# Performance work log

Measured on AMD Instinct MI355X. Metric: run time of the kernel, lower is better.

The kernel has to match this reference:

```python
import jax, jax.numpy as jnp
import numpy as np

N_A = 50000   # 'user' nodes
N_B = 50000   # 'item' nodes
E = 1000000   # edges per relation
IN, HID, OUT = 128, 128, 64


def setup_inputs() -> dict:
    key = jax.random.key(0)
    ks = jax.random.split(key, 24)
    def glorot(k, shape):
        scale = 1.0 / np.sqrt(shape[0])
        return jax.random.normal(k, shape, jnp.float32) * scale
    inp = {
        "feat_A": jax.random.normal(ks[0], (N_A, IN), jnp.float32),
        "feat_B": jax.random.normal(ks[1], (N_B, IN), jnp.float32),
        "rates_src": jax.random.randint(ks[2], (E,), 0, N_A, jnp.int32),
        "rates_dst": jax.random.randint(ks[3], (E,), 0, N_B, jnp.int32),
        "ratedby_src": jax.random.randint(ks[4], (E,), 0, N_B, jnp.int32),
        "ratedby_dst": jax.random.randint(ks[5], (E,), 0, N_A, jnp.int32),
        "follows_src": jax.random.randint(ks[6], (E,), 0, N_A, jnp.int32),
        "follows_dst": jax.random.randint(ks[7], (E,), 0, N_A, jnp.int32),
        "neg_src": jax.random.randint(ks[8], (E,), 0, N_A, jnp.int32),
        "neg_dst": jax.random.randint(ks[9], (E,), 0, N_B, jnp.int32),
        "W1_rates": glorot(ks[10], (IN, HID)),   "b1_rates": jnp.zeros((HID,), jnp.float32),
        "W1_ratedby": glorot(ks[11], (IN, HID)), "b1_ratedby": jnp.zeros((HID,), jnp.float32),
        "W1_follows": glorot(ks[12], (IN, HID)), "b1_follows": jnp.zeros((HID,), jnp.float32),
        "W2_rates": glorot(ks[13], (HID, OUT)),   "b2_rates": jnp.zeros((OUT,), jnp.float32),
        "W2_ratedby": glorot(ks[14], (HID, OUT)), "b2_ratedby": jnp.zeros((OUT,), jnp.float32),
        "W2_follows": glorot(ks[15], (HID, OUT)), "b2_follows": jnp.zeros((OUT,), jnp.float32),
    }
    return inp


def _graph_conv(x_src, W, b, src, dst, n_src, n_dst):
    # DGL GraphConv, norm='both': D_dst^{-1/2} A D_src^{-1/2} (X W) + b
    ones = jnp.ones(src.shape[0], x_src.dtype)
    deg_out = jnp.maximum(jax.ops.segment_sum(ones, src, num_segments=n_src), 1.0)
    deg_in = jnp.maximum(jax.ops.segment_sum(ones, dst, num_segments=n_dst), 1.0)
    h = (x_src * (deg_out ** -0.5)[:, None]) @ W          # [n_src, d_out]
    agg = jax.ops.segment_sum(h[src], dst, num_segments=n_dst)  # SpMM
    return agg * (deg_in ** -0.5)[:, None] + b


def reference(feat_A, feat_B,
              W1_rates, b1_rates, W1_ratedby, b1_ratedby, W1_follows, b1_follows,
              W2_rates, b2_rates, W2_ratedby, b2_ratedby, W2_follows, b2_follows,
              rates_src, rates_dst, ratedby_src, ratedby_dst,
              follows_src, follows_dst, neg_src, neg_dst):
    # --- RGCN layer 1 (HeteroGraphConv, aggregate='sum') ---
    hB = _graph_conv(feat_A, W1_rates, b1_rates, rates_src, rates_dst, N_A, N_B)
    hA = (_graph_conv(feat_B, W1_ratedby, b1_ratedby, ratedby_src, ratedby_dst, N_B, N_A)
          + _graph_conv(feat_A, W1_follows, b1_follows, follows_src, follows_dst, N_A, N_A))
    hA = jax.nn.relu(hA)
    hB = jax.nn.relu(hB)
    # --- RGCN layer 2 ---
    oB = _graph_conv(hA, W2_rates, b2_rates, rates_src, rates_dst, N_A, N_B)
    oA = (_graph_conv(hB, W2_ratedby, b2_ratedby, ratedby_src, ratedby_dst, N_B, N_A)
          + _graph_conv(hA, W2_follows, b2_follows, follows_src, follows_dst, N_A, N_A))
    # --- HeteroInnerProduct (u_dot_v on etype 'rates') for pos and neg graphs ---
    pos_score = jnp.sum(oA[rates_src] * oB[rates_dst], axis=1, keepdims=True)  # [E, 1]
    neg_score = jnp.sum(oA[neg_src] * oB[neg_dst], axis=1, keepdims=True)      # [E, 1]
    return pos_score, neg_score
```

## Files before the change

kernel.cpp:

```cpp
#include <hip/hip_runtime.h>
#include <hip/hip_fp16.h>
#include <cstddef>
#include <type_traits>

#define N_NODES 50000
#define E_EDGES 1000000
#define NBUCK 196
#define ACHUNK 3907
#define MTILES 3125
#define HB 96
#define HCHUNK 10417
#define GB1 384
#define GB2 256

typedef _Float16 f16x8 __attribute__((ext_vector_type(8)));
typedef float f32x4 __attribute__((ext_vector_type(4)));

__global__ __launch_bounds__(256) void fused0(
        const float* __restrict__ w0, const float* __restrict__ w1,
        const float* __restrict__ w2, const float* __restrict__ w3,
        const float* __restrict__ w4, const float* __restrict__ w5,
        __half* __restrict__ Wt,
        const int* __restrict__ rs, const int* __restrict__ rd,
        const int* __restrict__ bs, const int* __restrict__ bd,
        const int* __restrict__ fs, const int* __restrict__ fd,
        int* __restrict__ bphist) {
    int bx = blockIdx.x;
    if (bx < 6 * HB) {
        __shared__ int l[NBUCK];
        int arr = bx / HB, blk = bx % HB;
        const int* idx = arr == 0 ? rs : arr == 1 ? rd : arr == 2 ? bs
                       : arr == 3 ? bd : arr == 4 ? fs : fd;
        for (int b = threadIdx.x; b < NBUCK; b += 256) l[b] = 0;
        __syncthreads();
        int e0 = blk * HCHUNK;
        int e1 = e0 + HCHUNK; if (e1 > E_EDGES) e1 = E_EDGES;
        for (int i = e0 + threadIdx.x; i < e1; i += 256)
            atomicAdd(&l[((unsigned)idx[i]) >> 8], 1);
        __syncthreads();
        int* dst = bphist + (size_t)(arr * HB + blk) * NBUCK;
        for (int b = threadIdx.x; b < NBUCK; b += 256) dst[b] = l[b];
        return;
    }
    bx -= 6 * HB;
    int m = bx / 16, part = bx % 16;
    const float* W = m == 0 ? w0 : m == 1 ? w1 : m == 2 ? w2 : m == 3 ? w3 : m == 4 ? w4 : w5;
    __half* Tt = Wt + (m < 3 ? m * 16384 : 49152 + (m - 3) * 8192);
    int ncol = m < 3 ? 128 : 64;
    int tot = 128 * ncol;
    for (int i = part * 256 + threadIdx.x; i < tot; i += 16 * 256) {
        int n = i >> 7, k = i & 127;
        Tt[i] = __float2half(W[k * ncol + n]);
    }
}

__global__ void bucket_scan_par(const int* __restrict__ bphist, int* __restrict__ gbase,
                                int* __restrict__ gcur) {
    int arr = blockIdx.x;
    int t = threadIdx.x;
    int c = 0;
    if (t < NBUCK) {
        const int* p = bphist + (size_t)arr * HB * NBUCK + t;
#pragma unroll 8
        for (int blk = 0; blk < HB; blk++) c += p[(size_t)blk * NBUCK];
    }
    int lane = t & 63, wid = t >> 6;
    __shared__ int wsum[4];
    int v = c;
#pragma unroll
    for (int o = 1; o < 64; o <<= 1) { int u = __shfl_up(v, o); if (lane >= o) v += u; }
    if (lane == 63) wsum[wid] = v;
    __syncthreads();
    int base = 0;
    for (int ww = 0; ww < wid; ww++) base += wsum[ww];
    int excl = base + v - c;
    if (t < NBUCK) {
        gbase[arr * (NBUCK + 1) + t] = excl;
        gcur[arr * NBUCK + t] = excl;
    }
    if (t == 255) gbase[arr * (NBUCK + 1) + NBUCK] = base + v;
}

__global__ __launch_bounds__(256) void fused_bin(
        const int* __restrict__ rs, const int* __restrict__ rd,
        const int* __restrict__ bs, const int* __restrict__ bd,
        const int* __restrict__ fs, const int* __restrict__ fd,
        int* __restrict__ gcur, unsigned* __restrict__ pairs,
        unsigned char* __restrict__ sbytes) {
    int y = blockIdx.y;
    __shared__ int lcnt[NBUCK];
    __shared__ int lbase[NBUCK];
    int e0 = blockIdx.x * ACHUNK;
    int e1 = e0 + ACHUNK; if (e1 > E_EDGES) e1 = E_EDGES;
    for (int b = threadIdx.x; b < NBUCK; b += 256) lcnt[b] = 0;
    __syncthreads();
    if (y < 3) {
        int rel = y, arr = 2 * rel + 1;
        const int* src = rel == 0 ? rs : rel == 1 ? bs : fs;
        const int* dst = rel == 0 ? rd : rel == 1 ? bd : fd;
        for (int i = e0 + threadIdx.x; i < e1; i += 256)
            atomicAdd(&lcnt[((unsigned)dst[i]) >> 8], 1);
        __syncthreads();
        for (int b = threadIdx.x; b < NBUCK; b += 256) {
            lbase[b] = lcnt[b] ? atomicAdd(&gcur[arr * NBUCK + b], lcnt[b]) : 0;
            lcnt[b] = 0;
        }
        __syncthreads();
        unsigned* pp = pairs + (size_t)rel * E_EDGES;
        for (int i = e0 + threadIdx.x; i < e1; i += 256) {
            int d = dst[i];
            int b = ((unsigned)d) >> 8;
            int p = lbase[b] + atomicAdd(&lcnt[b], 1);
            pp[p] = ((unsigned)(d & 255) << 16) | (unsigned)src[i];
        }
    } else {
        int rel = y - 3, arr = 2 * rel;
        const int* src = rel == 0 ? rs : rel == 1 ? bs : fs;
        for (int i = e0 + threadIdx.x; i < e1; i += 256)
            atomicAdd(&lcnt[((unsigned)src[i]) >> 8], 1);
        __syncthreads();
        for (int b = threadIdx.x; b < NBUCK; b += 256) {
            lbase[b] = lcnt[b] ? atomicAdd(&gcur[arr * NBUCK + b], lcnt[b]) : 0;
            lcnt[b] = 0;
        }
        __syncthreads();
        unsigned char* sb = sbytes + (size_t)rel * E_EDGES;
        for (int i = e0 + threadIdx.x; i < e1; i += 256) {
            int s = src[i];
            int b = ((unsigned)s) >> 8;
            int p = lbase[b] + atomicAdd(&lcnt[b], 1);
            sb[p] = (unsigned char)(s & 255);
        }
    }
}

__global__ __launch_bounds__(256) void fused_finish(
        const unsigned* __restrict__ pairs, const unsigned char* __restrict__ sbytes,
        const int* __restrict__ gbase, int* __restrict__ row_ptr,
        float* __restrict__ scales, int* __restrict__ col) {
    int y = blockIdx.y, b = blockIdx.x, t = threadIdx.x;
    __shared__ int cnt[256];
    __shared__ int rowbase[256];
    __shared__ int wsum[4];
    if (y < 3) {
        int rel = y, arr = 2 * rel;
        int p0 = gbase[arr * (NBUCK + 1) + b];
        int p1 = gbase[arr * (NBUCK + 1) + b + 1];
        const unsigned char* sb = sbytes + (size_t)rel * E_EDGES;
        cnt[t] = 0;
        __syncthreads();
        for (int i = p0 + t; i < p1; i += 256)
            atomicAdd(&cnt[sb[i]], 1);
        __syncthreads();
        int node = b * 256 + t;
        if (node < N_NODES) {
            int c = cnt[t]; if (c < 1) c = 1;
            scales[(size_t)arr * N_NODES + node] = 1.0f / sqrtf((float)c);
        }
    } else {
        int rel = y - 3, arr = 2 * rel + 1;
        int gb = gbase[arr * (NBUCK + 1) + b];
        int ge = gbase[arr * (NBUCK + 1) + b + 1];
        const unsigned* pp = pairs + (size_t)rel * E_EDGES;
        cnt[t] = 0;
        __syncthreads();
        for (int i = gb + t; i < ge; i += 256)
            atomicAdd(&cnt[pp[i] >> 16], 1);
        __syncthreads();
        int lane = t & 63, wid = t >> 6;
        int c0 = cnt[t];
        int v = c0;
#pragma unroll
        for (int o = 1; o < 64; o <<= 1) { int u = __shfl_up(v, o); if (lane >= o) v += u; }
        if (lane == 63) wsum[wid] = v;
        __syncthreads();
        int base = gb;
        for (int w = 0; w < wid; w++) base += wsum[w];
        int excl = base + v - c0;
        rowbase[t] = excl;
        int node = b * 256 + t;
        if (node <= N_NODES)
            row_ptr[(size_t)rel * (N_NODES + 1) + node] = excl;
        if (node < N_NODES) {
            int c = c0; if (c < 1) c = 1;
            scales[(size_t)arr * N_NODES + node] = 1.0f / sqrtf((float)c);
        }
        cnt[t] = 0;
        __syncthreads();
        int* cl = col + (size_t)rel * E_EDGES;
        for (int i = gb + t; i < ge; i += 256) {
            unsigned p = pp[i];
            int dl = p >> 16;
            int slot = rowbase[dl] + atomicAdd(&cnt[dl], 1);
            cl[slot] = (int)(p & 0xFFFFu);
        }
    }
}

template <int NCOL, typename XT>
__device__ __forceinline__ void gemm_body(const XT* __restrict__ X,
                                          const float* __restrict__ sc,
                                          const __half* __restrict__ Wt,
                                          __half* __restrict__ T,
                                          int bxr, int nblocks) {
    constexpr int NHALF = NCOL / 64;
    int gw = bxr * 4 + ((int)threadIdx.x >> 6);
    int lane = threadIdx.x & 63;
    int half_id = gw % NHALF;
    int mstream = gw / NHALF;
    int nstreams = nblocks * 4 / NHALF;
    int l15 = lane & 15, g = lane >> 4;

    f16x8 b[4][4];
    {
        const __half* wb = Wt + ((size_t)half_id * 64 + l15) * 128 + g * 8;
#pragma unroll
        for (int nt = 0; nt < 4; nt++)
#pragma unroll
            for (int kb = 0; kb < 4; kb++)
                b[nt][kb] = *(const f16x8*)(wb + nt * 16 * 128 + kb * 32);
    }

    for (int mt = mstream; mt < MTILES; mt += nstreams) {
        int m0 = mt * 16;
        f16x8 a[4];
        if constexpr (std::is_same<XT, float>::value) {
            const float* xr = X + (size_t)(m0 + l15) * 128 + g * 8;
#pragma unroll
            for (int kb = 0; kb < 4; kb++) {
                float4 u = *(const float4*)(xr + kb * 32);
                float4 v = *(const float4*)(xr + kb * 32 + 4);
                f16x8 t;
                t[0] = (_Float16)u.x; t[1] = (_Float16)u.y;
                t[2] = (_Float16)u.z; t[3] = (_Float16)u.w;
                t[4] = (_Float16)v.x; t[5] = (_Float16)v.y;
                t[6] = (_Float16)v.z; t[7] = (_Float16)v.w;
                a[kb] = t;
            }
        } else {
            const _Float16* xr = (const _Float16*)X + (size_t)(m0 + l15) * 128 + g * 8;
#pragma unroll
            for (int kb = 0; kb < 4; kb++)
                a[kb] = *(const f16x8*)(xr + kb * 32);
        }
        f32x4 acc[4];
#pragma unroll
        for (int nt = 0; nt < 4; nt++) acc[nt] = (f32x4){0.f, 0.f, 0.f, 0.f};
#pragma unroll
        for (int kb = 0; kb < 4; kb++)
#pragma unroll
            for (int nt = 0; nt < 4; nt++)
                acc[nt] = __builtin_amdgcn_mfma_f32_16x16x32_f16(a[kb], b[nt][kb], acc[nt], 0, 0, 0);
        int mrow = m0 + g * 4;
#pragma unroll
        for (int j = 0; j < 4; j++) {
            float sj = sc[mrow + j];
            __half* tj = T + (size_t)(mrow + j) * NCOL + half_id * 64 + l15;
            tj[0]  = __float2half(acc[0][j] * sj);
            tj[16] = __float2half(acc[1][j] * sj);
            tj[32] = __float2half(acc[2][j] * sj);
            tj[48] = __float2half(acc[3][j] * sj);
        }
    }
}

__global__ __launch_bounds__(256) void gemm_l1(const float* __restrict__ fA,
                                               const float* __restrict__ fB,
                                               const float* __restrict__ scales,
                                               const __half* __restrict__ Wt,
                                               __half* __restrict__ T012) {
    int rel = blockIdx.x / GB1, bxr = blockIdx.x % GB1;
    const float* X = (rel == 1) ? fB : fA;
    const float* sc = scales + (rel == 0 ? 0 : rel == 1 ? 2 * N_NODES : 4 * N_NODES);
    const __half* W = Wt + rel * 16384;
    __half* T = T012 + (size_t)rel * N_NODES * 128;
    gemm_body<128, float>(X, sc, W, T, bxr, GB1);
}

__global__ __launch_bounds__(256) void gemm_l2(const __half* __restrict__ hA,
                                               const __half* __restrict__ hB,
                                               const float* __restrict__ scales,
                                               const __half* __restrict__ Wt,
                                               __half* __restrict__ Tp) {
    int rel = blockIdx.x / GB2, bxr = blockIdx.x % GB2;
    const __half* X = (rel == 1) ? hB : hA;
    const float* sc = scales + (rel == 0 ? 0 : rel == 1 ? 2 * N_NODES : 4 * N_NODES);
    const __half* W = Wt + 49152 + rel * 8192;
    __half* T = Tp + (size_t)rel * N_NODES * 64;
    gemm_body<64, __half>(X, sc, W, T, bxr, GB2);
}

__global__ __launch_bounds__(256) void spmm_l1(
        const int* __restrict__ row_ptr, const int* __restrict__ col,
        const __half* __restrict__ T012, const float* __restrict__ scales,
        const float* __restrict__ b1r, const float* __restrict__ b1rb,
        const float* __restrict__ b1f,
        __half* __restrict__ hB, __half* __restrict__ hA) {
    int w = (blockIdx.x * blockDim.x + threadIdx.x) >> 6;
    int lane = threadIdx.x & 63;
    unsigned loff = (unsigned)lane << 2;
    const char* T0 = (const char*)T012;
    const char* T1 = T0 + (size_t)N_NODES * 256;
    const char* T2 = T1 + (size_t)N_NODES * 256;
#define LDT(B, c) __half22float2(*(const __half2*)((B) + (((unsigned)(c) << 8) + loff)))
    if (w < N_NODES / 2) {
        const int* cl = col;
        int rowA = w * 2, rowB = rowA + 1;
        int eA = row_ptr[rowA], EA = row_ptr[rowA + 1];
        int eB = EA, EB = row_ptr[rowB + 1];
        float axA = 0.f, ayA = 0.f, axB = 0.f, ayB = 0.f;
        while (eA + 4 <= EA && eB + 4 <= EB) {
            int a0 = cl[eA], a1 = cl[eA+1], a2 = cl[eA+2], a3 = cl[eA+3];
            int b0 = cl[eB], b1 = cl[eB+1], b2 = cl[eB+2], b3 = cl[eB+3];
            float2 v0 = LDT(T0, a0), v1 = LDT(T0, a1), v2 = LDT(T0, a2), v3 = LDT(T0, a3);
            float2 u0 = LDT(T0, b0), u1 = LDT(T0, b1), u2 = LDT(T0, b2), u3 = LDT(T0, b3);
            axA += (v0.x + v1.x) + (v2.x + v3.x); ayA += (v0.y + v1.y) + (v2.y + v3.y);
            axB += (u0.x + u1.x) + (u2.x + u3.x); ayB += (u0.y + u1.y) + (u2.y + u3.y);
            eA += 4; eB += 4;
        }
        while (eA + 4 <= EA) {
            int a0 = cl[eA], a1 = cl[eA+1], a2 = cl[eA+2], a3 = cl[eA+3];
            float2 v0 = LDT(T0, a0), v1 = LDT(T0, a1), v2 = LDT(T0, a2), v3 = LDT(T0, a3);
            axA += (v0.x + v1.x) + (v2.x + v3.x); ayA += (v0.y + v1.y) + (v2.y + v3.y);
            eA += 4;
        }
        while (eB + 4 <= EB) {
            int b0 = cl[eB], b1 = cl[eB+1], b2 = cl[eB+2], b3 = cl[eB+3];
            float2 u0 = LDT(T0, b0), u1 = LDT(T0, b1), u2 = LDT(T0, b2), u3 = LDT(T0, b3);
            axB += (u0.x + u1.x) + (u2.x + u3.x); ayB += (u0.y + u1.y) + (u2.y + u3.y);
            eB += 4;
        }
        while (eA < EA && eB < EB) {
            float2 v = LDT(T0, cl[eA]), u = LDT(T0, cl[eB]);
            axA += v.x; ayA += v.y; axB += u.x; ayB += u.y;
            eA++; eB++;
        }
        for (; eA < EA; eA++) { float2 v = LDT(T0, cl[eA]); axA += v.x; ayA += v.y; }
        for (; eB < EB; eB++) { float2 v = LDT(T0, cl[eB]); axB += v.x; ayB += v.y; }
        float bx = b1r[2 * lane], by = b1r[2 * lane + 1];
        float sA = scales[N_NODES + rowA], sB = scales[N_NODES + rowB];
        float ox = fmaxf(fmaf(axA, sA, bx), 0.f), oy = fmaxf(fmaf(ayA, sA, by), 0.f);
        *(__half2*)(hB + (size_t)rowA * 128 + 2 * lane) = __floats2half2_rn(ox, oy);
        ox = fmaxf(fmaf(axB, sB, bx), 0.f); oy = fmaxf(fmaf(ayB, sB, by), 0.f);
        *(__half2*)(hB + (size_t)rowB * 128 + 2 * lane) = __floats2half2_rn(ox, oy);
    } else {
        int r = w - N_NODES / 2;
        const int* rp1 = row_ptr + (N_NODES + 1);
        const int* rp2 = row_ptr + 2 * (N_NODES + 1);
        const int* cl1 = col + E_EDGES;
        const int* cl2 = col + 2 * (size_t)E_EDGES;
        int e1 = rp1[r], E1 = rp1[r + 1];
        int e2 = rp2[r], E2 = rp2[r + 1];
        float a1x = 0.f, a1y = 0.f, a2x = 0.f, a2y = 0.f;
        while (e1 + 4 <= E1 && e2 + 4 <= E2) {
            int a0 = cl1[e1], a1 = cl1[e1+1], a2 = cl1[e1+2], a3 = cl1[e1+3];
            int b0 = cl2[e2], b1 = cl2[e2+1], b2 = cl2[e2+2], b3 = cl2[e2+3];
            float2 v0 = LDT(T1, a0), v1 = LDT(T1, a1), v2 = LDT(T1, a2), v3 = LDT(T1, a3);
            float2 u0 = LDT(T2, b0), u1 = LDT(T2, b1), u2 = LDT(T2, b2), u3 = LDT(T2, b3);
            a1x += (v0.x + v1.x) + (v2.x + v3.x); a1y += (v0.y + v1.y) + (v2.y + v3.y);
            a2x += (u0.x + u1.x) + (u2.x + u3.x); a2y += (u0.y + u1.y) + (u2.y + u3.y);
            e1 += 4; e2 += 4;
        }
        while (e1 + 4 <= E1) {
            int a0 = cl1[e1], a1 = cl1[e1+1], a2 = cl1[e1+2], a3 = cl1[e1+3];
            float2 v0 = LDT(T1, a0), v1 = LDT(T1, a1), v2 = LDT(T1, a2), v3 = LDT(T1, a3);
            a1x += (v0.x + v1.x) + (v2.x + v3.x); a1y += (v0.y + v1.y) + (v2.y + v3.y);
            e1 += 4;
        }
        while (e2 + 4 <= E2) {
            int b0 = cl2[e2], b1 = cl2[e2+1], b2 = cl2[e2+2], b3 = cl2[e2+3];
            float2 u0 = LDT(T2, b0), u1 = LDT(T2, b1), u2 = LDT(T2, b2), u3 = LDT(T2, b3);
            a2x += (u0.x + u1.x) + (u2.x + u3.x); a2y += (u0.y + u1.y) + (u2.y + u3.y);
            e2 += 4;
        }
        while (e1 < E1 && e2 < E2) {
            float2 v = LDT(T1, cl1[e1]), u = LDT(T2, cl2[e2]);
            a1x += v.x; a1y += v.y; a2x += u.x; a2y += u.y;
            e1++; e2++;
        }
        for (; e1 < E1; e1++) { float2 v = LDT(T1, cl1[e1]); a1x += v.x; a1y += v.y; }
        for (; e2 < E2; e2++) { float2 v = LDT(T2, cl2[e2]); a2x += v.x; a2y += v.y; }
        float s1 = scales[3 * N_NODES + r], s2 = scales[5 * N_NODES + r];
        float ox = a1x * s1 + a2x * s2 + b1rb[2 * lane] + b1f[2 * lane];
        float oy = a1y * s1 + a2y * s2 + b1rb[2 * lane + 1] + b1f[2 * lane + 1];
        ox = fmaxf(ox, 0.f); oy = fmaxf(oy, 0.f);
        *(__half2*)(hA + (size_t)r * 128 + 2 * lane) = __floats2half2_rn(ox, oy);
    }
#undef LDT
}

__global__ __launch_bounds__(256) void spmm_l2(
        const int* __restrict__ row_ptr, const int* __restrict__ col,
        const __half* __restrict__ Tp, const float* __restrict__ scales,
        const float* __restrict__ b2r, const float* __restrict__ b2rb,
        const float* __restrict__ b2f,
        __half* __restrict__ oB, __half* __restrict__ oA) {
    int g = (blockIdx.x * blockDim.x + threadIdx.x) >> 5;
    int l2 = threadIdx.x & 31;
    unsigned loff = (unsigned)l2 << 2;
    const char* T0 = (const char*)Tp;
    const char* T1 = T0 + (size_t)N_NODES * 128;
    const char* T2 = T1 + (size_t)N_NODES * 128;
#define LDT(B, c) __half22float2(*(const __half2*)((B) + (((unsigned)(c) << 7) + loff)))
    if (g < N_NODES / 2) {
        const int* cl = col;
        int rowA = g * 2, rowB = rowA + 1;
        int eA = row_ptr[rowA], EA = row_ptr[rowA + 1];
        int eB = EA, EB = row_ptr[rowB + 1];
        float axA = 0.f, ayA = 0.f, axB = 0.f, ayB = 0.f;
        while (eA + 4 <= EA && eB + 4 <= EB) {
            int a0 = cl[eA], a1 = cl[eA+1], a2 = cl[eA+2], a3 = cl[eA+3];
            int b0 = cl[eB], b1 = cl[eB+1], b2 = cl[eB+2], b3 = cl[eB+3];
            float2 v0 = LDT(T0, a0), v1 = LDT(T0, a1), v2 = LDT(T0, a2), v3 = LDT(T0, a3);
            float2 u0 = LDT(T0, b0), u1 = LDT(T0, b1), u2 = LDT(T0, b2), u3 = LDT(T0, b3);
            axA += (v0.x + v1.x) + (v2.x + v3.x); ayA += (v0.y + v1.y) + (v2.y + v3.y);
            axB += (u0.x + u1.x) + (u2.x + u3.x); ayB += (u0.y + u1.y) + (u2.y + u3.y);
            eA += 4; eB += 4;
        }
        while (eA + 4 <= EA) {
            int a0 = cl[eA], a1 = cl[eA+1], a2 = cl[eA+2], a3 = cl[eA+3];
            float2 v0 = LDT(T0, a0), v1 = LDT(T0, a1), v2 = LDT(T0, a2), v3 = LDT(T0, a3);
            axA += (v0.x + v1.x) + (v2.x + v3.x); ayA += (v0.y + v1.y) + (v2.y + v3.y);
            eA += 4;
        }
        while (eB + 4 <= EB) {
            int b0 = cl[eB], b1 = cl[eB+1], b2 = cl[eB+2], b3 = cl[eB+3];
            float2 u0 = LDT(T0, b0), u1 = LDT(T0, b1), u2 = LDT(T0, b2), u3 = LDT(T0, b3);
            axB += (u0.x + u1.x) + (u2.x + u3.x); ayB += (u0.y + u1.y) + (u2.y + u3.y);
            eB += 4;
        }
        while (eA < EA && eB < EB) {
            float2 v = LDT(T0, cl[eA]), u = LDT(T0, cl[eB]);
            axA += v.x; ayA += v.y; axB += u.x; ayB += u.y;
            eA++; eB++;
        }
        for (; eA < EA; eA++) { float2 v = LDT(T0, cl[eA]); axA += v.x; ayA += v.y; }
        for (; eB < EB; eB++) { float2 v = LDT(T0, cl[eB]); axB += v.x; ayB += v.y; }
        float bx = b2r[2 * l2], by = b2r[2 * l2 + 1];
        float sA = scales[N_NODES + rowA], sB = scales[N_NODES + rowB];
        *(__half2*)(oB + (size_t)rowA * 64 + 2 * l2) =
            __floats2half2_rn(fmaf(axA, sA, bx), fmaf(ayA, sA, by));
        *(__half2*)(oB + (size_t)rowB * 64 + 2 * l2) =
            __floats2half2_rn(fmaf(axB, sB, bx), fmaf(ayB, sB, by));
    } else {
        int r = g - N_NODES / 2;
        const int* rp1 = row_ptr + (N_NODES + 1);
        const int* rp2 = row_ptr + 2 * (N_NODES + 1);
        const int* cl1 = col + E_EDGES;
        const int* cl2 = col + 2 * (size_t)E_EDGES;
        int e1 = rp1[r], E1 = rp1[r + 1];
        int e2 = rp2[r], E2 = rp2[r + 1];
        float a1x = 0.f, a1y = 0.f, a2x = 0.f, a2y = 0.f;
        while (e1 + 4 <= E1 && e2 + 4 <= E2) {
            int a0 = cl1[e1], a1 = cl1[e1+1], a2 = cl1[e1+2], a3 = cl1[e1+3];
            int b0 = cl2[e2], b1 = cl2[e2+1], b2 = cl2[e2+2], b3 = cl2[e2+3];
            float2 v0 = LDT(T1, a0), v1 = LDT(T1, a1), v2 = LDT(T1, a2), v3 = LDT(T1, a3);
            float2 u0 = LDT(T2, b0), u1 = LDT(T2, b1), u2 = LDT(T2, b2), u3 = LDT(T2, b3);
            a1x += (v0.x + v1.x) + (v2.x + v3.x); a1y += (v0.y + v1.y) + (v2.y + v3.y);
            a2x += (u0.x + u1.x) + (u2.x + u3.x); a2y += (u0.y + u1.y) + (u2.y + u3.y);
            e1 += 4; e2 += 4;
        }
        while (e1 + 4 <= E1) {
            int a0 = cl1[e1], a1 = cl1[e1+1], a2 = cl1[e1+2], a3 = cl1[e1+3];
            float2 v0 = LDT(T1, a0), v1 = LDT(T1, a1), v2 = LDT(T1, a2), v3 = LDT(T1, a3);
            a1x += (v0.x + v1.x) + (v2.x + v3.x); a1y += (v0.y + v1.y) + (v2.y + v3.y);
            e1 += 4;
        }
        while (e2 + 4 <= E2) {
            int b0 = cl2[e2], b1 = cl2[e2+1], b2 = cl2[e2+2], b3 = cl2[e2+3];
            float2 u0 = LDT(T2, b0), u1 = LDT(T2, b1), u2 = LDT(T2, b2), u3 = LDT(T2, b3);
            a2x += (u0.x + u1.x) + (u2.x + u3.x); a2y += (u0.y + u1.y) + (u2.y + u3.y);
            e2 += 4;
        }
        while (e1 < E1 && e2 < E2) {
            float2 v = LDT(T1, cl1[e1]), u = LDT(T2, cl2[e2]);
            a1x += v.x; a1y += v.y; a2x += u.x; a2y += u.y;
            e1++; e2++;
        }
        for (; e1 < E1; e1++) { float2 v = LDT(T1, cl1[e1]); a1x += v.x; a1y += v.y; }
        for (; e2 < E2; e2++) { float2 v = LDT(T2, cl2[e2]); a2x += v.x; a2y += v.y; }
        float s1 = scales[3 * N_NODES + r], s2 = scales[5 * N_NODES + r];
        float ox = a1x * s1 + a2x * s2 + b2rb[2 * l2] + b2f[2 * l2];
        float oy = a1y * s1 + a2y * s2 + b2rb[2 * l2 + 1] + b2f[2 * l2 + 1];
        *(__half2*)(oA + (size_t)r * 64 + 2 * l2) = __floats2half2_rn(ox, oy);
    }
#undef LDT
}

__global__ __launch_bounds__(256) void score2(const __half* __restrict__ oA,
                                              const __half* __restrict__ oB,
                                              const int* __restrict__ ps,
                                              const int* __restrict__ pd,
                                              const int* __restrict__ ns,
                                              const int* __restrict__ nd,
                                              float* __restrict__ out) {
    int g = (blockIdx.x * blockDim.x + threadIdx.x) >> 4;
    int l = threadIdx.x & 15;
    int ng = (gridDim.x * blockDim.x) >> 4;
    const char* A = (const char*)oA;
    const char* B = (const char*)oB;
    unsigned loff = (unsigned)l << 3;
#define SCORE_LOOP(SRC, DST, OUT)                                               \
    for (int e0 = g * 2; e0 < E_EDGES; e0 += ng * 2) {                          \
        int e1 = e0 + 1;                                                        \
        int s0 = SRC[e0], d0 = DST[e0], s1 = SRC[e1], d1 = DST[e1];             \
        union { uint2 u; __half2 h[2]; } a0, b0, a1, b1;                        \
        a0.u = *(const uint2*)(A + (((unsigned)s0 << 7) + loff));               \
        b0.u = *(const uint2*)(B + (((unsigned)d0 << 7) + loff));               \
        a1.u = *(const uint2*)(A + (((unsigned)s1 << 7) + loff));               \
        b1.u = *(const uint2*)(B + (((unsigned)d1 << 7) + loff));               \
        float2 fa, fb;                                                          \
        fa = __half22float2(a0.h[0]); fb = __half22float2(b0.h[0]);             \
        float p0 = fa.x * fb.x + fa.y * fb.y;                                   \
        fa = __half22float2(a0.h[1]); fb = __half22float2(b0.h[1]);             \
        p0 += fa.x * fb.x + fa.y * fb.y;                                        \
        fa = __half22float2(a1.h[0]); fb = __half22float2(b1.h[0]);             \
        float p1 = fa.x * fb.x + fa.y * fb.y;                                   \
        fa = __half22float2(a1.h[1]); fb = __half22float2(b1.h[1]);             \
        p1 += fa.x * fb.x + fa.y * fb.y;                                        \
        p0 += __shfl_xor(p0, 8); p1 += __shfl_xor(p1, 8);                       \
        p0 += __shfl_xor(p0, 4); p1 += __shfl_xor(p1, 4);                       \
        p0 += __shfl_xor(p0, 2); p1 += __shfl_xor(p1, 2);                       \
        p0 += __shfl_xor(p0, 1); p1 += __shfl_xor(p1, 1);                       \
        if (l == 0) { OUT[e0] = p0; OUT[e1] = p1; }                             \
    }
    SCORE_LOOP(ps, pd, out)
    float* outn = out + E_EDGES;
    SCORE_LOOP(ns, nd, outn)
#undef SCORE_LOOP
}

extern "C" void kernel_launch(void* const* d_in, const int* in_sizes, int n_in,
                              void* d_out, int out_size, void* d_ws, size_t ws_size,
                              hipStream_t stream) {
    const float* feat_A     = (const float*)d_in[0];
    const float* feat_B     = (const float*)d_in[1];
    const int* rates_src    = (const int*)d_in[2];
    const int* rates_dst    = (const int*)d_in[3];
    const int* ratedby_src  = (const int*)d_in[4];
    const int* ratedby_dst  = (const int*)d_in[5];
    const int* follows_src  = (const int*)d_in[6];
    const int* follows_dst  = (const int*)d_in[7];
    const int* neg_src      = (const int*)d_in[8];
    const int* neg_dst      = (const int*)d_in[9];
    const float* W1_rates   = (const float*)d_in[10];
    const float* b1_rates   = (const float*)d_in[11];
    const float* W1_ratedby = (const float*)d_in[12];
    const float* b1_ratedby = (const float*)d_in[13];
    const float* W1_follows = (const float*)d_in[14];
    const float* b1_follows = (const float*)d_in[15];
    const float* W2_rates   = (const float*)d_in[16];
    const float* b2_rates   = (const float*)d_in[17];
    const float* W2_ratedby = (const float*)d_in[18];
    const float* b2_ratedby = (const float*)d_in[19];
    const float* W2_follows = (const float*)d_in[20];
    const float* b2_follows = (const float*)d_in[21];

    const int N = N_NODES, E = E_EDGES;

    char* ws = (char*)d_ws;
    size_t off = 0;
    auto alloc = [&](size_t bytes) -> void* {
        void* p = ws + off;
        off += (bytes + 255) & ~(size_t)255;
        return p;
    };
    float* scales = (float*)alloc((size_t)6 * N * 4);
    int* row_ptr  = (int*)alloc((size_t)3 * (N + 1) * 4);
    int* bphist   = (int*)alloc((size_t)6 * HB * NBUCK * 4);
    int* gbase    = (int*)alloc((size_t)6 * (NBUCK + 1) * 4);
    int* gcur     = (int*)alloc((size_t)6 * NBUCK * 4);
    int* col      = (int*)alloc((size_t)3 * E * 4);
    unsigned* pairs = (unsigned*)alloc((size_t)3 * E * 4);
    unsigned char* sbytes = (unsigned char*)alloc((size_t)3 * E);
    __half* T012  = (__half*)alloc((size_t)3 * N * 128 * 2);
    __half* Tp    = (__half*)alloc((size_t)3 * N * 64 * 2);
    __half* hA    = (__half*)alloc((size_t)N * 128 * 2);
    __half* hB    = (__half*)alloc((size_t)N * 128 * 2);
    __half* oA    = (__half*)alloc((size_t)N * 64 * 2);
    __half* oB    = (__half*)alloc((size_t)N * 64 * 2);
    __half* Wt    = (__half*)alloc((size_t)(3 * 128 * 128 + 3 * 128 * 64) * 2);
    (void)ws_size;

    fused0<<<6 * HB + 96, 256, 0, stream>>>(W1_rates, W1_ratedby, W1_follows,
                                            W2_rates, W2_ratedby, W2_follows, Wt,
                                            rates_src, rates_dst, ratedby_src,
                                            ratedby_dst, follows_src, follows_dst,
                                            bphist);
    bucket_scan_par<<<6, 256, 0, stream>>>(bphist, gbase, gcur);
    fused_bin<<<dim3(256, 6), 256, 0, stream>>>(rates_src, rates_dst, ratedby_src,
                                                ratedby_dst, follows_src, follows_dst,
                                                gcur, pairs, sbytes);
    fused_finish<<<dim3(NBUCK, 6), 256, 0, stream>>>(pairs, sbytes, gbase,
                                                     row_ptr, scales, col);

    gemm_l1<<<3 * GB1, 256, 0, stream>>>(feat_A, feat_B, scales, Wt, T012);
    spmm_l1<<<(3 * N / 2) / 4, 256, 0, stream>>>(row_ptr, col, T012, scales,
                                                 b1_rates, b1_ratedby, b1_follows,
                                                 hB, hA);
    gemm_l2<<<3 * GB2, 256, 0, stream>>>(hA, hB, scales, Wt, Tp);
    spmm_l2<<<(3 * N / 2) / 8, 256, 0, stream>>>(row_ptr, col, Tp, scales,
                                                 b2_rates, b2_ratedby, b2_follows,
                                                 oB, oA);
    score2<<<8192, 256, 0, stream>>>(oA, oB, rates_src, rates_dst,
                                     neg_src, neg_dst, (float*)d_out);
}
```

Baseline: 358.9 us.

## Interleave relation work across blocks with persistent grid-stride SpMM loops

Both SpMM kernels now launch a fixed-size grid and use grid-stride loops, with blocks split into 8 slots: 3 handle the 'rates' row pairs and 5 handle the combined 'ratedby'+'follows' rows. Previously the first third of blocks did rates and the rest did A-side rows in launch order. The change mixes the two workloads across the GPU at the same time and balances them by their relative cost. It also cuts the number of block launches. The cost is fewer waves and possible tail imbalance if the 3:5 ratio does not match the actual per-row costs.

```diff
diff --git a/kernel.cpp b/kernel.cpp
--- a/kernel.cpp
+++ b/kernel.cpp
@@ -12,6 +12,8 @@
 #define HCHUNK 10417
 #define GB1 384
 #define GB2 256
+#define SLB1 256
+#define SLB2 128
 
 typedef _Float16 f16x8 __attribute__((ext_vector_type(8)));
 typedef float f32x4 __attribute__((ext_vector_type(4)));
@@ -296,95 +298,100 @@
         const float* __restrict__ b1r, const float* __restrict__ b1rb,
         const float* __restrict__ b1f,
         __half* __restrict__ hB, __half* __restrict__ hA) {
-    int w = (blockIdx.x * blockDim.x + threadIdx.x) >> 6;
+    int slot = blockIdx.x & 7;
+    int w = (blockIdx.x >> 3) * 4 + ((int)threadIdx.x >> 6);
+    const int NW = SLB1 * 4;
     int lane = threadIdx.x & 63;
     unsigned loff = (unsigned)lane << 2;
     const char* T0 = (const char*)T012;
     const char* T1 = T0 + (size_t)N_NODES * 256;
     const char* T2 = T1 + (size_t)N_NODES * 256;
 #define LDT(B, c) __half22float2(*(const __half2*)((B) + (((unsigned)(c) << 8) + loff)))
-    if (w < N_NODES / 2) {
-        const int* cl = col;
-        int rowA = w * 2, rowB = rowA + 1;
-        int eA = row_ptr[rowA], EA = row_ptr[rowA + 1];
-        int eB = EA, EB = row_ptr[rowB + 1];
-        float axA = 0.f, ayA = 0.f, axB = 0.f, ayB = 0.f;
-        while (eA + 4 <= EA && eB + 4 <= EB) {
-            int a0 = cl[eA], a1 = cl[eA+1], a2 = cl[eA+2], a3 = cl[eA+3];
-            int b0 = cl[eB], b1 = cl[eB+1], b2 = cl[eB+2], b3 = cl[eB+3];
-            float2 v0 = LDT(T0, a0), v1 = LDT(T0, a1), v2 = LDT(T0, a2), v3 = LDT(T0, a3);
-            float2 u0 = LDT(T0, b0), u1 = LDT(T0, b1), u2 = LDT(T0, b2), u3 = LDT(T0, b3);
-            axA += (v0.x + v1.x) + (v2.x + v3.x); ayA += (v0.y + v1.y) + (v2.y + v3.y);
-            axB += (u0.x + u1.x) + (u2.x + u3.x); ayB += (u0.y + u1.y) + (u2.y + u3.y);
-            eA += 4; eB += 4;
-        }
-        while (eA + 4 <= EA) {
-            int a0 = cl[eA], a1 = cl[eA+1], a2 = cl[eA+2], a3 = cl[eA+3];
-            float2 v0 = LDT(T0, a0), v1 = LDT(T0, a1), v2 = LDT(T0, a2), v3 = LDT(T0, a3);
-            axA += (v0.x + v1.x) + (v2.x + v3.x); ayA += (v0.y + v1.y) + (v2.y + v3.y);
-            eA += 4;
-        }
-        while (eB + 4 <= EB) {
-            int b0 = cl[eB], b1 = cl[eB+1], b2 = cl[eB+2], b3 = cl[eB+3];
-            float2 u0 = LDT(T0, b0), u1 = LDT(T0, b1), u2 = LDT(T0, b2), u3 = LDT(T0, b3);
-            axB += (u0.x + u1.x) + (u2.x + u3.x); ayB += (u0.y + u1.y) + (u2.y + u3.y);
-            eB += 4;
-        }
-        while (eA < EA && eB < EB) {
-            float2 v = LDT(T0, cl[eA]), u = LDT(T0, cl[eB]);
-            axA += v.x; ayA += v.y; axB += u.x; ayB += u.y;
-            eA++; eB++;
-        }
-        for (; eA < EA; eA++) { float2 v = LDT(T0, cl[eA]); axA += v.x; ayA += v.y; }
-        for (; eB < EB; eB++) { float2 v = LDT(T0, cl[eB]); axB += v.x; ayB += v.y; }
-        float bx = b1r[2 * lane], by = b1r[2 * lane + 1];
-        float sA = scales[N_NODES + rowA], sB = scales[N_NODES + rowB];
-        float ox = fmaxf(fmaf(axA, sA, bx), 0.f), oy = fmaxf(fmaf(ayA, sA, by), 0.f);
-        *(__half2*)(hB + (size_t)rowA * 128 + 2 * lane) = __floats2half2_rn(ox, oy);
-        ox = fmaxf(fmaf(axB, sB, bx), 0.f); oy = fmaxf(fmaf(ayB, sB, by), 0.f);
-        *(__half2*)(hB + (size_t)rowB * 128 + 2 * lane) = __floats2half2_rn(ox, oy);
+    if (slot < 3) {
+        for (int p = slot + 3 * w; p < N_NODES / 2; p += 3 * NW) {
+            const int* cl = col;
+            int rowA = p * 2, rowB = rowA + 1;
+            int eA = row_ptr[rowA], EA = row_ptr[rowA + 1];
+            int eB = EA, EB = row_ptr[rowB + 1];
+            float axA = 0.f, ayA = 0.f, axB = 0.f, ayB = 0.f;
+            while (eA + 4 <= EA && eB + 4 <= EB) {
+                int a0 = cl[eA], a1 = cl[eA+1], a2 = cl[eA+2], a3 = cl[eA+3];
+                int b0 = cl[eB], b1 = cl[eB+1], b2 = cl[eB+2], b3 = cl[eB+3];
+                float2 v0 = LDT(T0, a0), v1 = LDT(T0, a1), v2 = LDT(T0, a2), v3 = LDT(T0, a3);
+                float2 u0 = LDT(T0, b0), u1 = LDT(T0, b1), u2 = LDT(T0, b2), u3 = LDT(T0, b3);
+                axA += (v0.x + v1.x) + (v2.x + v3.x); ayA += (v0.y + v1.y) + (v2.y + v3.y);
+                axB += (u0.x + u1.x) + (u2.x + u3.x); ayB += (u0.y + u1.y) + (u2.y + u3.y);
+                eA += 4; eB += 4;
+            }
+            while (eA + 4 <= EA) {
+                int a0 = cl[eA], a1 = cl[eA+1], a2 = cl[eA+2], a3 = cl[eA+3];
+                float2 v0 = LDT(T0, a0), v1 = LDT(T0, a1), v2 = LDT(T0, a2), v3 = LDT(T0, a3);
+                axA += (v0.x + v1.x) + (v2.x + v3.x); ayA += (v0.y + v1.y) + (v2.y + v3.y);
+                eA += 4;
+            }
+            while (eB + 4 <= EB) {
+                int b0 = cl[eB], b1 = cl[eB+1], b2 = cl[eB+2], b3 = cl[eB+3];
+                float2 u0 = LDT(T0, b0), u1 = LDT(T0, b1), u2 = LDT(T0, b2), u3 = LDT(T0, b3);
+                axB += (u0.x + u1.x) + (u2.x + u3.x); ayB += (u0.y + u1.y) + (u2.y + u3.y);
+                eB += 4;
+            }
+            while (eA < EA && eB < EB) {
+                float2 v = LDT(T0, cl[eA]), u = LDT(T0, cl[eB]);
+                axA += v.x; ayA += v.y; axB += u.x; ayB += u.y;
+                eA++; eB++;
+            }
+            for (; eA < EA; eA++) { float2 v = LDT(T0, cl[eA]); axA += v.x; ayA += v.y; }
+            for (; eB < EB; eB++) { float2 v = LDT(T0, cl[eB]); axB += v.x; ayB += v.y; }
+            float bx = b1r[2 * lane], by = b1r[2 * lane + 1];
+            float sA = scales[N_NODES + rowA], sB = scales[N_NODES + rowB];
+            float ox = fmaxf(fmaf(axA, sA, bx), 0.f), oy = fmaxf(fmaf(ayA, sA, by), 0.f);
+            *(__half2*)(hB + (size_t)rowA * 128 + 2 * lane) = __floats2half2_rn(ox, oy);
+            ox = fmaxf(fmaf(axB, sB, bx), 0.f); oy = fmaxf(fmaf(ayB, sB, by), 0.f);
+            *(__half2*)(hB + (size_t)rowB * 128 + 2 * lane) = __floats2half2_rn(ox, oy);
+        }
     } else {
-        int r = w - N_NODES / 2;
         const int* rp1 = row_ptr + (N_NODES + 1);
         const int* rp2 = row_ptr + 2 * (N_NODES + 1);
         const int* cl1 = col + E_EDGES;
         const int* cl2 = col + 2 * (size_t)E_EDGES;
-        int e1 = rp1[r], E1 = rp1[r + 1];
-        int e2 = rp2[r], E2 = rp2[r + 1];
-        float a1x = 0.f, a1y = 0.f, a2x = 0.f, a2y = 0.f;
-        while (e1 + 4 <= E1 && e2 + 4 <= E2) {
-            int a0 = cl1[e1], a1 = cl1[e1+1], a2 = cl1[e1+2], a3 = cl1[e1+3];
-            int b0 = cl2[e2], b1 = cl2[e2+1], b2 = cl2[e2+2], b3 = cl2[e2+3];
-            float2 v0 = LDT(T1, a0), v1 = LDT(T1, a1), v2 = LDT(T1, a2), v3 = LDT(T1, a3);
-            float2 u0 = LDT(T2, b0), u1 = LDT(T2, b1), u2 = LDT(T2, b2), u3 = LDT(T2, b3);
-            a1x += (v0.x + v1.x) + (v2.x + v3.x); a1y += (v0.y + v1.y) + (v2.y + v3.y);
-            a2x += (u0.x + u1.x) + (u2.x + u3.x); a2y += (u0.y + u1.y) + (u2.y + u3.y);
-            e1 += 4; e2 += 4;
-        }
-        while (e1 + 4 <= E1) {
-            int a0 = cl1[e1], a1 = cl1[e1+1], a2 = cl1[e1+2], a3 = cl1[e1+3];
-            float2 v0 = LDT(T1, a0), v1 = LDT(T1, a1), v2 = LDT(T1, a2), v3 = LDT(T1, a3);
-            a1x += (v0.x + v1.x) + (v2.x + v3.x); a1y += (v0.y + v1.y) + (v2.y + v3.y);
-            e1 += 4;
-        }
-        while (e2 + 4 <= E2) {
-            int b0 = cl2[e2], b1 = cl2[e2+1], b2 = cl2[e2+2], b3 = cl2[e2+3];
-            float2 u0 = LDT(T2, b0), u1 = LDT(T2, b1), u2 = LDT(T2, b2), u3 = LDT(T2, b3);
-            a2x += (u0.x + u1.x) + (u2.x + u3.x); a2y += (u0.y + u1.y) + (u2.y + u3.y);
-            e2 += 4;
-        }
-        while (e1 < E1 && e2 < E2) {
-            float2 v = LDT(T1, cl1[e1]), u = LDT(T2, cl2[e2]);
-            a1x += v.x; a1y += v.y; a2x += u.x; a2y += u.y;
-            e1++; e2++;
-        }
-        for (; e1 < E1; e1++) { float2 v = LDT(T1, cl1[e1]); a1x += v.x; a1y += v.y; }
-        for (; e2 < E2; e2++) { float2 v = LDT(T2, cl2[e2]); a2x += v.x; a2y += v.y; }
-        float s1 = scales[3 * N_NODES + r], s2 = scales[5 * N_NODES + r];
-        float ox = a1x * s1 + a2x * s2 + b1rb[2 * lane] + b1f[2 * lane];
-        float oy = a1y * s1 + a2y * s2 + b1rb[2 * lane + 1] + b1f[2 * lane + 1];
-        ox = fmaxf(ox, 0.f); oy = fmaxf(oy, 0.f);
-        *(__half2*)(hA + (size_t)r * 128 + 2 * lane) = __floats2half2_rn(ox, oy);
+        for (int r = (slot - 3) + 5 * w; r < N_NODES; r += 5 * NW) {
+            int e1 = rp1[r], E1 = rp1[r + 1];
+            int e2 = rp2[r], E2 = rp2[r + 1];
+            float a1x = 0.f, a1y = 0.f, a2x = 0.f, a2y = 0.f;
+            while (e1 + 4 <= E1 && e2 + 4 <= E2) {
+                int a0 = cl1[e1], a1 = cl1[e1+1], a2 = cl1[e1+2], a3 = cl1[e1+3];
+                int b0 = cl2[e2], b1 = cl2[e2+1], b2 = cl2[e2+2], b3 = cl2[e2+3];
+                float2 v0 = LDT(T1, a0), v1 = LDT(T1, a1), v2 = LDT(T1, a2), v3 = LDT(T1, a3);
+                float2 u0 = LDT(T2, b0), u1 = LDT(T2, b1), u2 = LDT(T2, b2), u3 = LDT(T2, b3);
+                a1x += (v0.x + v1.x) + (v2.x + v3.x); a1y += (v0.y + v1.y) + (v2.y + v3.y);
+                a2x += (u0.x + u1.x) + (u2.x + u3.x); a2y += (u0.y + u1.y) + (u2.y + u3.y);
+                e1 += 4; e2 += 4;
+            }
+            while (e1 + 4 <= E1) {
+                int a0 = cl1[e1], a1 = cl1[e1+1], a2 = cl1[e1+2], a3 = cl1[e1+3];
+                float2 v0 = LDT(T1, a0), v1 = LDT(T1, a1), v2 = LDT(T1, a2), v3 = LDT(T1, a3);
+                a1x += (v0.x + v1.x) + (v2.x + v3.x); a1y += (v0.y + v1.y) + (v2.y + v3.y);
+                e1 += 4;
+            }
+            while (e2 + 4 <= E2) {
+                int b0 = cl2[e2], b1 = cl2[e2+1], b2 = cl2[e2+2], b3 = cl2[e2+3];
+                float2 u0 = LDT(T2, b0), u1 = LDT(T2, b1), u2 = LDT(T2, b2), u3 = LDT(T2, b3);
+                a2x += (u0.x + u1.x) + (u2.x + u3.x); a2y += (u0.y + u1.y) + (u2.y + u3.y);
+                e2 += 4;
+            }
+            while (e1 < E1 && e2 < E2) {
+                float2 v = LDT(T1, cl1[e1]), u = LDT(T2, cl2[e2]);
+                a1x += v.x; a1y += v.y; a2x += u.x; a2y += u.y;
+                e1++; e2++;
+            }
+            for (; e1 < E1; e1++) { float2 v = LDT(T1, cl1[e1]); a1x += v.x; a1y += v.y; }
+            for (; e2 < E2; e2++) { float2 v = LDT(T2, cl2[e2]); a2x += v.x; a2y += v.y; }
+            float s1 = scales[3 * N_NODES + r], s2 = scales[5 * N_NODES + r];
+            float ox = a1x * s1 + a2x * s2 + b1rb[2 * lane] + b1f[2 * lane];
+            float oy = a1y * s1 + a2y * s2 + b1rb[2 * lane + 1] + b1f[2 * lane + 1];
+            ox = fmaxf(ox, 0.f); oy = fmaxf(oy, 0.f);
+            *(__half2*)(hA + (size_t)r * 128 + 2 * lane) = __floats2half2_rn(ox, oy);
+        }
     }
 #undef LDT
 }
@@ -395,94 +402,99 @@
         const float* __restrict__ b2r, const float* __restrict__ b2rb,
         const float* __restrict__ b2f,
         __half* __restrict__ oB, __half* __restrict__ oA) {
-    int g = (blockIdx.x * blockDim.x + threadIdx.x) >> 5;
+    int slot = blockIdx.x & 7;
+    int g = (blockIdx.x >> 3) * 8 + ((int)threadIdx.x >> 5);
+    const int NG = SLB2 * 8;
     int l2 = threadIdx.x & 31;
     unsigned loff = (unsigned)l2 << 2;
     const char* T0 = (const char*)Tp;
     const char* T1 = T0 + (size_t)N_NODES * 128;
     const char* T2 = T1 + (size_t)N_NODES * 128;
 #define LDT(B, c) __half22float2(*(const __half2*)((B) + (((unsigned)(c) << 7) + loff)))
-    if (g < N_NODES / 2) {
-        const int* cl = col;
-        int rowA = g * 2, rowB = rowA + 1;
-        int eA = row_ptr[rowA], EA = row_ptr[rowA + 1];
-        int eB = EA, EB = row_ptr[rowB + 1];
-        float axA = 0.f, ayA = 0.f, axB = 0.f, ayB = 0.f;
-        while (eA + 4 <= EA && eB + 4 <= EB) {
-            int a0 = cl[eA], a1 = cl[eA+1], a2 = cl[eA+2], a3 = cl[eA+3];
-            int b0 = cl[eB], b1 = cl[eB+1], b2 = cl[eB+2], b3 = cl[eB+3];
-            float2 v0 = LDT(T0, a0), v1 = LDT(T0, a1), v2 = LDT(T0, a2), v3 = LDT(T0, a3);
-            float2 u0 = LDT(T0, b0), u1 = LDT(T0, b1), u2 = LDT(T0, b2), u3 = LDT(T0, b3);
-            axA += (v0.x + v1.x) + (v2.x + v3.x); ayA += (v0.y + v1.y) + (v2.y + v3.y);
-            axB += (u0.x + u1.x) + (u2.x + u3.x); ayB += (u0.y + u1.y) + (u2.y + u3.y);
-            eA += 4; eB += 4;
-        }
-        while (eA + 4 <= EA) {
-            int a0 = cl[eA], a1 = cl[eA+1], a2 = cl[eA+2], a3 = cl[eA+3];
-            float2 v0 = LDT(T0, a0), v1 = LDT(T0, a1), v2 = LDT(T0, a2), v3 = LDT(T0, a3);
-            axA += (v0.x + v1.x) + (v2.x + v3.x); ayA += (v0.y + v1.y) + (v2.y + v3.y);
-            eA += 4;
-        }
-        while (eB + 4 <= EB) {
-            int b0 = cl[eB], b1 = cl[eB+1], b2 = cl[eB+2], b3 = cl[eB+3];
-            float2 u0 = LDT(T0, b0), u1 = LDT(T0, b1), u2 = LDT(T0, b2), u3 = LDT(T0, b3);
-            axB += (u0.x + u1.x) + (u2.x + u3.x); ayB += (u0.y + u1.y) + (u2.y + u3.y);
-            eB += 4;
-        }
-        while (eA < EA && eB < EB) {
-            float2 v = LDT(T0, cl[eA]), u = LDT(T0, cl[eB]);
-            axA += v.x; ayA += v.y; axB += u.x; ayB += u.y;
-            eA++; eB++;
-        }
-        for (; eA < EA; eA++) { float2 v = LDT(T0, cl[eA]); axA += v.x; ayA += v.y; }
-        for (; eB < EB; eB++) { float2 v = LDT(T0, cl[eB]); axB += v.x; ayB += v.y; }
-        float bx = b2r[2 * l2], by = b2r[2 * l2 + 1];
-        float sA = scales[N_NODES + rowA], sB = scales[N_NODES + rowB];
-        *(__half2*)(oB + (size_t)rowA * 64 + 2 * l2) =
-            __floats2half2_rn(fmaf(axA, sA, bx), fmaf(ayA, sA, by));
-        *(__half2*)(oB + (size_t)rowB * 64 + 2 * l2) =
-            __floats2half2_rn(fmaf(axB, sB, bx), fmaf(ayB, sB, by));
+    if (slot < 3) {
+        for (int p = slot + 3 * g; p < N_NODES / 2; p += 3 * NG) {
+            const int* cl = col;
+            int rowA = p * 2, rowB = rowA + 1;
+            int eA = row_ptr[rowA], EA = row_ptr[rowA + 1];
+            int eB = EA, EB = row_ptr[rowB + 1];
+            float axA = 0.f, ayA = 0.f, axB = 0.f, ayB = 0.f;
+            while (eA + 4 <= EA && eB + 4 <= EB) {
+                int a0 = cl[eA], a1 = cl[eA+1], a2 = cl[eA+2], a3 = cl[eA+3];
+                int b0 = cl[eB], b1 = cl[eB+1], b2 = cl[eB+2], b3 = cl[eB+3];
+                float2 v0 = LDT(T0, a0), v1 = LDT(T0, a1), v2 = LDT(T0, a2), v3 = LDT(T0, a3);
+                float2 u0 = LDT(T0, b0), u1 = LDT(T0, b1), u2 = LDT(T0, b2), u3 = LDT(T0, b3);
+                axA += (v0.x + v1.x) + (v2.x + v3.x); ayA += (v0.y + v1.y) + (v2.y + v3.y);
+                axB += (u0.x + u1.x) + (u2.x + u3.x); ayB += (u0.y + u1.y) + (u2.y + u3.y);
+                eA += 4; eB += 4;
+            }
+            while (eA + 4 <= EA) {
+                int a0 = cl[eA], a1 = cl[eA+1], a2 = cl[eA+2], a3 = cl[eA+3];
+                float2 v0 = LDT(T0, a0), v1 = LDT(T0, a1), v2 = LDT(T0, a2), v3 = LDT(T0, a3);
+                axA += (v0.x + v1.x) + (v2.x + v3.x); ayA += (v0.y + v1.y) + (v2.y + v3.y);
+                eA += 4;
+            }
+            while (eB + 4 <= EB) {
+                int b0 = cl[eB], b1 = cl[eB+1], b2 = cl[eB+2], b3 = cl[eB+3];
+                float2 u0 = LDT(T0, b0), u1 = LDT(T0, b1), u2 = LDT(T0, b2), u3 = LDT(T0, b3);
+                axB += (u0.x + u1.x) + (u2.x + u3.x); ayB += (u0.y + u1.y) + (u2.y + u3.y);
+                eB += 4;
+            }
+            while (eA < EA && eB < EB) {
+                float2 v = LDT(T0, cl[eA]), u = LDT(T0, cl[eB]);
+                axA += v.x; ayA += v.y; axB += u.x; ayB += u.y;
+                eA++; eB++;
+            }
+            for (; eA < EA; eA++) { float2 v = LDT(T0, cl[eA]); axA += v.x; ayA += v.y; }
+            for (; eB < EB; eB++) { float2 v = LDT(T0, cl[eB]); axB += v.x; ayB += v.y; }
+            float bx = b2r[2 * l2], by = b2r[2 * l2 + 1];
+            float sA = scales[N_NODES + rowA], sB = scales[N_NODES + rowB];
+            *(__half2*)(oB + (size_t)rowA * 64 + 2 * l2) =
+                __floats2half2_rn(fmaf(axA, sA, bx), fmaf(ayA, sA, by));
+            *(__half2*)(oB + (size_t)rowB * 64 + 2 * l2) =
+                __floats2half2_rn(fmaf(axB, sB, bx), fmaf(ayB, sB, by));
+        }
     } else {
-        int r = g - N_NODES / 2;
         const int* rp1 = row_ptr + (N_NODES + 1);
         const int* rp2 = row_ptr + 2 * (N_NODES + 1);
         const int* cl1 = col + E_EDGES;
         const int* cl2 = col + 2 * (size_t)E_EDGES;
-        int e1 = rp1[r], E1 = rp1[r + 1];
-        int e2 = rp2[r], E2 = rp2[r + 1];
-        float a1x = 0.f, a1y = 0.f, a2x = 0.f, a2y = 0.f;
-        while (e1 + 4 <= E1 && e2 + 4 <= E2) {
-            int a0 = cl1[e1], a1 = cl1[e1+1], a2 = cl1[e1+2], a3 = cl1[e1+3];
-            int b0 = cl2[e2], b1 = cl2[e2+1], b2 = cl2[e2+2], b3 = cl2[e2+3];
-            float2 v0 = LDT(T1, a0), v1 = LDT(T1, a1), v2 = LDT(T1, a2), v3 = LDT(T1, a3);
-            float2 u0 = LDT(T2, b0), u1 = LDT(T2, b1), u2 = LDT(T2, b2), u3 = LDT(T2, b3);
-            a1x += (v0.x + v1.x) + (v2.x + v3.x); a1y += (v0.y + v1.y) + (v2.y + v3.y);
-            a2x += (u0.x + u1.x) + (u2.x + u3.x); a2y += (u0.y + u1.y) + (u2.y + u3.y);
-            e1 += 4; e2 += 4;
-        }
-        while (e1 + 4 <= E1) {
-            int a0 = cl1[e1], a1 = cl1[e1+1], a2 = cl1[e1+2], a3 = cl1[e1+3];
-            float2 v0 = LDT(T1, a0), v1 = LDT(T1, a1), v2 = LDT(T1, a2), v3 = LDT(T1, a3);
-            a1x += (v0.x + v1.x) + (v2.x + v3.x); a1y += (v0.y + v1.y) + (v2.y + v3.y);
-            e1 += 4;
-        }
-        while (e2 + 4 <= E2) {
-            int b0 = cl2[e2], b1 = cl2[e2+1], b2 = cl2[e2+2], b3 = cl2[e2+3];
-            float2 u0 = LDT(T2, b0), u1 = LDT(T2, b1), u2 = LDT(T2, b2), u3 = LDT(T2, b3);
-            a2x += (u0.x + u1.x) + (u2.x + u3.x); a2y += (u0.y + u1.y) + (u2.y + u3.y);
-            e2 += 4;
-        }
-        while (e1 < E1 && e2 < E2) {
-            float2 v = LDT(T1, cl1[e1]), u = LDT(T2, cl2[e2]);
-            a1x += v.x; a1y += v.y; a2x += u.x; a2y += u.y;
-            e1++; e2++;
-        }
-        for (; e1 < E1; e1++) { float2 v = LDT(T1, cl1[e1]); a1x += v.x; a1y += v.y; }
-        for (; e2 < E2; e2++) { float2 v = LDT(T2, cl2[e2]); a2x += v.x; a2y += v.y; }
-        float s1 = scales[3 * N_NODES + r], s2 = scales[5 * N_NODES + r];
-        float ox = a1x * s1 + a2x * s2 + b2rb[2 * l2] + b2f[2 * l2];
-        float oy = a1y * s1 + a2y * s2 + b2rb[2 * l2 + 1] + b2f[2 * l2 + 1];
-        *(__half2*)(oA + (size_t)r * 64 + 2 * l2) = __floats2half2_rn(ox, oy);
+        for (int r = (slot - 3) + 5 * g; r < N_NODES; r += 5 * NG) {
+            int e1 = rp1[r], E1 = rp1[r + 1];
+            int e2 = rp2[r], E2 = rp2[r + 1];
+            float a1x = 0.f, a1y = 0.f, a2x = 0.f, a2y = 0.f;
+            while (e1 + 4 <= E1 && e2 + 4 <= E2) {
+                int a0 = cl1[e1], a1 = cl1[e1+1], a2 = cl1[e1+2], a3 = cl1[e1+3];
+                int b0 = cl2[e2], b1 = cl2[e2+1], b2 = cl2[e2+2], b3 = cl2[e2+3];
+                float2 v0 = LDT(T1, a0), v1 = LDT(T1, a1), v2 = LDT(T1, a2), v3 = LDT(T1, a3);
+                float2 u0 = LDT(T2, b0), u1 = LDT(T2, b1), u2 = LDT(T2, b2), u3 = LDT(T2, b3);
+                a1x += (v0.x + v1.x) + (v2.x + v3.x); a1y += (v0.y + v1.y) + (v2.y + v3.y);
+                a2x += (u0.x + u1.x) + (u2.x + u3.x); a2y += (u0.y + u1.y) + (u2.y + u3.y);
+                e1 += 4; e2 += 4;
+            }
+            while (e1 + 4 <= E1) {
+                int a0 = cl1[e1], a1 = cl1[e1+1], a2 = cl1[e1+2], a3 = cl1[e1+3];
+                float2 v0 = LDT(T1, a0), v1 = LDT(T1, a1), v2 = LDT(T1, a2), v3 = LDT(T1, a3);
+                a1x += (v0.x + v1.x) + (v2.x + v3.x); a1y += (v0.y + v1.y) + (v2.y + v3.y);
+                e1 += 4;
+            }
+            while (e2 + 4 <= E2) {
+                int b0 = cl2[e2], b1 = cl2[e2+1], b2 = cl2[e2+2], b3 = cl2[e2+3];
+                float2 u0 = LDT(T2, b0), u1 = LDT(T2, b1), u2 = LDT(T2, b2), u3 = LDT(T2, b3);
+                a2x += (u0.x + u1.x) + (u2.x + u3.x); a2y += (u0.y + u1.y) + (u2.y + u3.y);
+                e2 += 4;
+            }
+            while (e1 < E1 && e2 < E2) {
+                float2 v = LDT(T1, cl1[e1]), u = LDT(T2, cl2[e2]);
+                a1x += v.x; a1y += v.y; a2x += u.x; a2y += u.y;
+                e1++; e2++;
+            }
+            for (; e1 < E1; e1++) { float2 v = LDT(T1, cl1[e1]); a1x += v.x; a1y += v.y; }
+            for (; e2 < E2; e2++) { float2 v = LDT(T2, cl2[e2]); a2x += v.x; a2y += v.y; }
+            float s1 = scales[3 * N_NODES + r], s2 = scales[5 * N_NODES + r];
+            float ox = a1x * s1 + a2x * s2 + b2rb[2 * l2] + b2f[2 * l2];
+            float oy = a1y * s1 + a2y * s2 + b2rb[2 * l2 + 1] + b2f[2 * l2 + 1];
+            *(__half2*)(oA + (size_t)r * 64 + 2 * l2) = __floats2half2_rn(ox, oy);
+        }
     }
 #undef LDT
 }
@@ -595,13 +607,13 @@
                                                      row_ptr, scales, col);
 
     gemm_l1<<<3 * GB1, 256, 0, stream>>>(feat_A, feat_B, scales, Wt, T012);
-    spmm_l1<<<(3 * N / 2) / 4, 256, 0, stream>>>(row_ptr, col, T012, scales,
-                                                 b1_rates, b1_ratedby, b1_follows,
-                                                 hB, hA);
+    spmm_l1<<<8 * SLB1, 256, 0, stream>>>(row_ptr, col, T012, scales,
+                                          b1_rates, b1_ratedby, b1_follows,
+                                          hB, hA);
     gemm_l2<<<3 * GB2, 256, 0, stream>>>(hA, hB, scales, Wt, Tp);
-    spmm_l2<<<(3 * N / 2) / 8, 256, 0, stream>>>(row_ptr, col, Tp, scales,
-                                                 b2_rates, b2_ratedby, b2_follows,
-                                                 oB, oA);
+    spmm_l2<<<8 * SLB2, 256, 0, stream>>>(row_ptr, col, Tp, scales,
+                                          b2_rates, b2_ratedby, b2_follows,
+                                          oB, oA);
     score2<<<8192, 256, 0, stream>>>(oA, oB, rates_src, rates_dst,
                                      neg_src, neg_dst, (float*)d_out);
 }
```

After: 404.7 us. +12.8%, slower.
